# Kernel tuning notes

Hardware: AMD Instinct MI355X
Metric: run time of the kernel (lower is better)

The kernel has to match this reference:

```python
import jax, jax.numpy as jnp
import numpy as np

B, T, D, NH = 4, 2048, 768, 12
DH = D // NH
NEG = -100000.0  # module uses masked_fill with -100000.0, not -inf


def setup_inputs() -> dict:
    key = jax.random.key(0)
    ks = jax.random.split(key, 9)
    s = 1.0 / np.sqrt(D)
    return {
        "x": jax.random.normal(ks[0], (B, T, D), jnp.float32),
        "wq": jax.random.normal(ks[1], (D, D), jnp.float32) * s,
        "bq": jax.random.normal(ks[2], (D,), jnp.float32) * 0.02,
        "wk": jax.random.normal(ks[3], (D, D), jnp.float32) * s,
        "bk": jax.random.normal(ks[4], (D,), jnp.float32) * 0.02,
        "wv": jax.random.normal(ks[5], (D, D), jnp.float32) * s,
        "bv": jax.random.normal(ks[6], (D,), jnp.float32) * 0.02,
        "wo": jax.random.normal(ks[7], (D, D), jnp.float32) * s,
        "bo": jax.random.normal(ks[8], (D,), jnp.float32) * 0.02,
    }


def reference(x, wq, bq, wk, bk, wv, bv, wo, bo):
    Bx, Tx, E = x.shape
    # torch Linear: y = x @ W.T + b, weight shape [out, in]
    def heads(w, b):
        return (x @ w.T + b).reshape(Bx, Tx, NH, DH).transpose(0, 2, 1, 3)  # [B,nh,T,dh]
    Q, K, V = heads(wq, bq), heads(wk, bk), heads(wv, bv)
    scale = 1.0 / jnp.sqrt(jnp.float32(DH))
    QK = jnp.einsum("bhqd,bhkd->bhqk", Q, K) * scale  # [B,nh,T,T]
    causal = jnp.tril(jnp.ones((Tx, Tx), dtype=bool))
    QK = jnp.where(causal, QK, NEG)
    A = jax.nn.softmax(QK, axis=-1)  # attn_dropout p=0 (eval)
    Z = jnp.einsum("bhqk,bhkd->bhqd", A, V)
    Z = Z.transpose(0, 2, 1, 3).reshape(Bx, Tx, E)
    return Z @ wo.T + bo  # resid_dropout p=0 (eval)
```

## Files before the change

kernel.cpp:

```cpp
#include <hip/hip_runtime.h>


#define B_ 4
#define T_ 2048
#define D_ 768
#define NH_ 12
#define DH_ 64
#define M_ (B_ * T_)

typedef __attribute__((ext_vector_type(8))) short bf16x8;
typedef __attribute__((ext_vector_type(4))) float f32x4;
typedef __attribute__((ext_vector_type(16))) float f32x16;
typedef __attribute__((ext_vector_type(4))) unsigned int u32x4;

__device__ __forceinline__ unsigned short f2bf(float f) {
  unsigned int u = __builtin_bit_cast(unsigned int, f);
  u += 0x7FFFu + ((u >> 16) & 1u);
  return (unsigned short)(u >> 16);
}

__device__ __forceinline__ void async16(const void* g, void* l) {
  __builtin_amdgcn_global_load_lds(
      (const __attribute__((address_space(1))) unsigned int*)g,
      (__attribute__((address_space(3))) unsigned int*)l, 16, 0, 0);
}

#define RAW_BARRIER()                         \
  do {                                        \
    asm volatile("" ::: "memory");            \
    __builtin_amdgcn_s_barrier();             \
    asm volatile("" ::: "memory");            \
  } while (0)

__global__ void cvt_kernel(const float* __restrict__ x, const float* __restrict__ wq,
                           const float* __restrict__ wk, const float* __restrict__ wv,
                           const float* __restrict__ wo,
                           unsigned short* __restrict__ xb, unsigned short* __restrict__ wqb,
                           unsigned short* __restrict__ wkb, unsigned short* __restrict__ wvb,
                           unsigned short* __restrict__ wob) {
  const float* src; unsigned short* dst; int n4;
  switch (blockIdx.y) {
    case 0: src = x;  dst = xb;  n4 = M_ * D_ / 4; break;
    case 1: src = wq; dst = wqb; n4 = D_ * D_ / 4; break;
    case 2: src = wk; dst = wkb; n4 = D_ * D_ / 4; break;
    case 3: src = wv; dst = wvb; n4 = D_ * D_ / 4; break;
    default: src = wo; dst = wob; n4 = D_ * D_ / 4; break;
  }
  int stride = gridDim.x * blockDim.x;
  for (int i = blockIdx.x * blockDim.x + threadIdx.x; i < n4; i += stride) {
    float4 v = ((const float4*)src)[i];
    ushort4 o;
    o.x = f2bf(v.x); o.y = f2bf(v.y); o.z = f2bf(v.z); o.w = f2bf(v.w);
    ((ushort4*)dst)[i] = o;
  }
}

__global__ __launch_bounds__(512, 4) void gemm_kernel(
    const unsigned short* __restrict__ A,
    const unsigned short* __restrict__ W0, const unsigned short* __restrict__ W1,
    const unsigned short* __restrict__ W2,
    const float* __restrict__ bias0, const float* __restrict__ bias1,
    const float* __restrict__ bias2,
    void* out0, void* out1, void* out2,
    float s0, int K, int qkv) {
  __shared__ __align__(16) char lds[73728];

  int bid = blockIdx.x;
  int xcd = bid & 7, g = bid >> 3;
  int mt, nt;
  if (qkv) { mt = xcd + (g / 9) * 8; nt = g % 9; }
  else     { mt = xcd + (g / 3) * 8; nt = g % 3; }
  int y  = qkv ? nt / 3 : 0;
  int nW = qkv ? nt % 3 : nt;
  const unsigned short* W = y == 0 ? W0 : (y == 1 ? W1 : W2);
  const float* bias = y == 0 ? bias0 : (y == 1 ? bias1 : bias2);
  void* outp = y == 0 ? out0 : (y == 1 ? out1 : out2);
  float scl = (qkv && y == 0) ? s0 : 1.0f;
  int mode = qkv ? ((y == 2) ? 2 : 1) : 0;

  int tid = threadIdx.x, lane = tid & 63, wid = tid >> 6;
  int l15 = lane & 15, l4 = lane >> 4;
  int wm = wid >> 2, wn = wid & 3;
  int m0 = mt << 7, n0w = nW << 8;

  int aRow, aCol;
  {
    int row = wid * 16 + (lane >> 2);
    int colE = (lane & 3) * 8;
    aRow = row;
    aCol = colE ^ (((row >> 1) & 3) << 3);
  }
  int bRow[2], bCol[2];
#pragma unroll
  for (int c = 0; c < 2; ++c) {
    int u = c * 8 + wid;
    int row = u * 16 + (lane >> 2);
    int colE = (lane & 3) * 8;
    bRow[c] = row;
    bCol[c] = colE ^ (((row >> 1) & 3) << 3);
  }

  int aoff[4], boff[4];
#pragma unroll
  for (int mf = 0; mf < 4; ++mf) {
    int row = wm * 64 + mf * 16 + l15;
    aoff[mf] = row * 64 + ((l4 * 16) ^ (((row >> 1) & 3) << 4));
  }
#pragma unroll
  for (int nf = 0; nf < 4; ++nf) {
    int row = wn * 64 + nf * 16 + l15;
    boff[nf] = 8192 + row * 64 + ((l4 * 16) ^ (((row >> 1) & 3) << 4));
  }

  const unsigned short* Wb = W + (size_t)n0w * K;

#define ISSUE_TILE(kt, slot)                                                       \
  do {                                                                             \
    async16(A + (size_t)(m0 + aRow) * K + (kt) + aCol, (slot) + wid * 1024);       \
    _Pragma("unroll") for (int c = 0; c < 2; ++c)                                  \
      async16(Wb + (size_t)bRow[c] * K + (kt) + bCol[c],                           \
              (slot) + 8192 + (c * 8 + wid) * 1024);                               \
  } while (0)

  f32x4 acc[4][4] = {};
  char* b0 = lds;
  char* b1 = lds + 24576;
  char* b2 = lds + 49152;

  ISSUE_TILE(0, b0);
  ISSUE_TILE(32, b1);

  int NT = K >> 5;
#pragma unroll 1
  for (int t = 0; t < NT; ++t) {
    if (t + 1 < NT) asm volatile("s_waitcnt vmcnt(3)" ::: "memory");
    else            asm volatile("s_waitcnt vmcnt(0)" ::: "memory");
    RAW_BARRIER();
    if (t + 2 < NT) ISSUE_TILE((t + 2) << 5, b2);
    bf16x8 af[4], bfr[4];
#pragma unroll
    for (int mf = 0; mf < 4; ++mf) af[mf] = *(const bf16x8*)(b0 + aoff[mf]);
#pragma unroll
    for (int nf = 0; nf < 4; ++nf) bfr[nf] = *(const bf16x8*)(b0 + boff[nf]);
    __builtin_amdgcn_s_setprio(1);
#pragma unroll
    for (int mf = 0; mf < 4; ++mf)
#pragma unroll
      for (int nf = 0; nf < 4; ++nf)
        acc[mf][nf] = __builtin_amdgcn_mfma_f32_16x16x32_bf16(af[mf], bfr[nf], acc[mf][nf], 0, 0, 0);
    __builtin_amdgcn_s_setprio(0);
    char* tmp = b0; b0 = b1; b1 = b2; b2 = tmp;
  }
#undef ISSUE_TILE

  if (mode == 2) {
#pragma unroll
    for (int nf = 0; nf < 4; ++nf) {
      int colW = n0w + wn * 64 + nf * 16 + l15;
      float bv = bias[colW];
      int h = colW >> 6, d = colW & 63;
#pragma unroll
      for (int mf = 0; mf < 4; ++mf) {
        int rbase = m0 + wm * 64 + mf * 16 + l4 * 4;
        int bb = rbase >> 11, tt = rbase & (T_ - 1);
        ushort4 o;
        o.x = f2bf(acc[mf][nf][0] + bv);
        o.y = f2bf(acc[mf][nf][1] + bv);
        o.z = f2bf(acc[mf][nf][2] + bv);
        o.w = f2bf(acc[mf][nf][3] + bv);
        *(ushort4*)((unsigned short*)outp + ((size_t)(bb * NH_ + h) * DH_ + d) * T_ + tt) = o;
      }
    }
  } else {
#pragma unroll
    for (int nf = 0; nf < 4; ++nf) {
      int colW = n0w + wn * 64 + nf * 16 + l15;
      float bv = bias[colW];
#pragma unroll
      for (int mf = 0; mf < 4; ++mf) {
        int rbase = m0 + wm * 64 + mf * 16 + l4 * 4;
#pragma unroll
        for (int r = 0; r < 4; ++r) {
          float v = (acc[mf][nf][r] + bv) * scl;
          size_t idx = (size_t)(rbase + r) * D_ + colW;
          if (mode == 1) ((unsigned short*)outp)[idx] = f2bf(v);
          else           ((float*)outp)[idx] = v;
        }
      }
    }
  }
}

__global__ __launch_bounds__(256, 2) void attn_kernel(
    const unsigned short* __restrict__ Q, const unsigned short* __restrict__ Kg,
    const unsigned short* __restrict__ VT, unsigned short* __restrict__ Z) {
  __shared__ __align__(16) char lds[57344];

  int tid = threadIdx.x, lane = tid & 63, w = tid >> 6;
  int l31 = lane & 31, hi = lane >> 5;
  int bid = blockIdx.x;
  int xcd = bid & 7, g = bid >> 3;
  int qt = 15 - g / 6;
  int bh = xcd + (g % 6) * 8;
  int b = bh / NH_, h = bh % NH_;
  int q0 = qt * 128;
  int qrow = q0 + w * 32 + l31;

  const unsigned short* Qb = Q + (size_t)(b * T_) * D_ + h * DH_;
  const unsigned short* Kb = Kg + (size_t)(b * T_) * D_ + h * DH_;
  const unsigned short* VTb = VT + (size_t)(b * NH_ + h) * DH_ * T_;

  bf16x8 qf[4];
#pragma unroll
  for (int s = 0; s < 4; ++s)
    qf[s] = *(const bf16x8*)(Qb + (size_t)qrow * D_ + s * 16 + hi * 8);

  int sRow[2], sCol[2];
#pragma unroll
  for (int c = 0; c < 2; ++c) {
    int pos = ((c * 4 + w) * 64 + lane) * 8;
    int row = pos >> 6, colE = pos & 63;
    sRow[c] = row;
    sCol[c] = colE ^ ((row & 7) << 3);
  }

  int koff[2][4];
#pragma unroll
  for (int n = 0; n < 2; ++n)
#pragma unroll
    for (int s = 0; s < 4; ++s) {
      int row = n * 32 + l31;
      koff[n][s] = row * 128 + ((s * 32 + hi * 16) ^ ((row & 7) << 4));
    }

  f32x16 zt[2] = {};
  float l_run = 0.f;
  int ntiles = 2 * qt + 2;

#pragma unroll
  for (int c = 0; c < 2; ++c) {
    async16(Kb + (size_t)sRow[c] * D_ + sCol[c], lds + 0 + (c * 4 + w) * 1024);
    async16(VTb + (size_t)sRow[c] * T_ + sCol[c], lds + 16384 + (c * 4 + w) * 1024);
  }

#define ATTN_TILE(KCUR, VCUR, KNXT, VNXT)                                              \
  do {                                                                                 \
    __syncthreads();          \
    if (t + 1 < ntiles) {                                                              \
      int kv1 = (t + 1) * 64;                                                          \
      _Pragma("unroll") for (int c = 0; c < 2; ++c) {                                  \
        async16(Kb + (size_t)(kv1 + sRow[c]) * D_ + sCol[c],                           \
                lds + KNXT + (c * 4 + w) * 1024);                                      \
        async16(VTb + (size_t)sRow[c] * T_ + kv1 + sCol[c],                            \
                lds + VNXT + (c * 4 + w) * 1024);                                      \
      }                                                                                \
    }                                                                                  \
    f32x16 st[2];                                                                      \
    __builtin_amdgcn_s_setprio(1);                                                     \
    _Pragma("unroll") for (int n = 0; n < 2; ++n) {                                    \
      f32x16 a = {};                                                                   \
      _Pragma("unroll") for (int s = 0; s < 4; ++s) {                                  \
        bf16x8 kf = *(const bf16x8*)(lds + KCUR + koff[n][s]);                         \
        a = __builtin_amdgcn_mfma_f32_32x32x16_bf16(kf, qf[s], a, 0, 0, 0);            \
      }                                                                                \
      st[n] = a;                                                                       \
    }                                                                                  \
    __builtin_amdgcn_s_setprio(0);                                                     \
    if (t >= 2 * qt) {                            \
      int kvb = t * 64;                                                                \
      _Pragma("unroll") for (int n = 0; n < 2; ++n)                                    \
        _Pragma("unroll") for (int m = 0; m < 4; ++m)                                  \
          _Pragma("unroll") for (int c2 = 0; c2 < 4; ++c2) {                           \
            int kv = kvb + n * 32 + m * 8 + hi * 4 + c2;                               \
            if (kv > qrow) st[n][m * 4 + c2] = -1e30f;                                 \
          }                                                                            \
    }                                                                                  \
    bf16x8 pb[4];                                                                      \
    _Pragma("unroll") for (int n = 0; n < 2; ++n) {                                    \
      float u[16];                                                                     \
      _Pragma("unroll") for (int r = 0; r < 16; ++r) {                                 \
        u[r] = __builtin_amdgcn_exp2f(st[n][r]);                                       \
        l_run += u[r];                                                                 \
      }                                                                                \
      _Pragma("unroll") for (int hf = 0; hf < 2; ++hf) {                               \
        unsigned int A0, A1, B0, B1;                                                   \
        asm("v_cvt_pk_bf16_f32 %0, %1, %2" : "=v"(A0) : "v"(u[hf*8+0]), "v"(u[hf*8+1]));\
        asm("v_cvt_pk_bf16_f32 %0, %1, %2" : "=v"(A1) : "v"(u[hf*8+2]), "v"(u[hf*8+3]));\
        asm("v_cvt_pk_bf16_f32 %0, %1, %2" : "=v"(B0) : "v"(u[hf*8+4]), "v"(u[hf*8+5]));\
        asm("v_cvt_pk_bf16_f32 %0, %1, %2" : "=v"(B1) : "v"(u[hf*8+6]), "v"(u[hf*8+7]));\
        asm("v_permlane32_swap_b32 %0, %1" : "+v"(A0), "+v"(B0));                      \
        asm("v_permlane32_swap_b32 %0, %1" : "+v"(A1), "+v"(B1));                      \
        u32x4 pk; pk[0] = A0; pk[1] = A1; pk[2] = B0; pk[3] = B1;                      \
        pb[n * 2 + hf] = __builtin_bit_cast(bf16x8, pk);                               \
      }                                                                                \
    }                                                                                  \
    __builtin_amdgcn_s_setprio(1);                                                     \
    _Pragma("unroll") for (int dt = 0; dt < 2; ++dt) {                                 \
      _Pragma("unroll") for (int s = 0; s < 4; ++s) {                                  \
        bf16x8 vf = *(const bf16x8*)(lds + VCUR + koff[dt][s]);                        \
        zt[dt] = __builtin_amdgcn_mfma_f32_32x32x16_bf16(vf, pb[s], zt[dt], 0, 0, 0);  \
      }                                                                                \
    }                                                                                  \
    __builtin_amdgcn_s_setprio(0);                                                     \
  } while (0)

#pragma unroll 1
  for (int t = 0; t < ntiles; ++t) {
    if ((t & 1) == 0) {
      ATTN_TILE(0, 16384, 8192, 24576);
    } else {
      ATTN_TILE(8192, 24576, 0, 16384);
    }
  }
#undef ATTN_TILE

  l_run += __shfl_xor(l_run, 32);
  float inv = __builtin_amdgcn_rcpf(l_run);
  unsigned short* Zrow = Z + (size_t)(b * T_ + qrow) * D_ + h * DH_;
#pragma unroll
  for (int dt = 0; dt < 2; ++dt)
#pragma unroll
    for (int m = 0; m < 4; ++m) {
      ushort4 o;
      o.x = f2bf(zt[dt][m * 4 + 0] * inv);
      o.y = f2bf(zt[dt][m * 4 + 1] * inv);
      o.z = f2bf(zt[dt][m * 4 + 2] * inv);
      o.w = f2bf(zt[dt][m * 4 + 3] * inv);
      *(ushort4*)(Zrow + dt * 32 + m * 8 + hi * 4) = o;
    }
}

extern "C" void kernel_launch(void* const* d_in, const int* in_sizes, int n_in,
                              void* d_out, int out_size, void* d_ws, size_t ws_size,
                              hipStream_t stream) {
  (void)in_sizes; (void)n_in; (void)out_size; (void)ws_size;
  const float* x  = (const float*)d_in[0];
  const float* wq = (const float*)d_in[1];
  const float* bq = (const float*)d_in[2];
  const float* wk = (const float*)d_in[3];
  const float* bk = (const float*)d_in[4];
  const float* wv = (const float*)d_in[5];
  const float* bv = (const float*)d_in[6];
  const float* wo = (const float*)d_in[7];
  const float* bo = (const float*)d_in[8];

  char* ws = (char*)d_ws;
  const size_t XB = (size_t)M_ * D_ * 2;
  const size_t WB = (size_t)D_ * D_ * 2;
  unsigned short* xb  = (unsigned short*)(ws);
  unsigned short* wqb = (unsigned short*)(ws + XB);
  unsigned short* wkb = (unsigned short*)(ws + XB + WB);
  unsigned short* wvb = (unsigned short*)(ws + XB + 2 * WB);
  unsigned short* wob = (unsigned short*)(ws + XB + 3 * WB);
  unsigned short* Qb  = (unsigned short*)(ws + XB + 4 * WB);
  unsigned short* Kb  = (unsigned short*)(ws + XB + 4 * WB + XB);
  unsigned short* VTb = (unsigned short*)(ws + XB + 4 * WB + 2 * XB);
  unsigned short* Zb  = xb;

  const float SCALE_Q = 0.125f * 1.44269504f;

  cvt_kernel<<<dim3(1024, 5), 256, 0, stream>>>(x, wq, wk, wv, wo, xb, wqb, wkb, wvb, wob);
  gemm_kernel<<<dim3(576), 512, 0, stream>>>(
      xb, wqb, wkb, wvb, bq, bk, bv, Qb, Kb, VTb, SCALE_Q, D_, 1);
  attn_kernel<<<dim3(768), 256, 0, stream>>>(Qb, Kb, VTb, Zb);
  gemm_kernel<<<dim3(192), 512, 0, stream>>>(
      Zb, wob, wob, wob, bo, bo, bo, d_out, d_out, d_out, 1.0f, D_, 0);
}
```

Baseline: 117.1 us.

## Load GEMM weight fragments directly to registers, double-buffer only A in LDS

The GEMM now stages only the activation tile in LDS with two buffers instead of three, and each wave loads its weight (B) fragments straight from global memory into registers, double-buffered across k-steps. This cuts LDS use from 72KB to 16KB and drops the launch_bounds minimum-occupancy hint. The aim is to save LDS bandwidth and shared-memory capacity, allowing more blocks per CU. In exchange, the weight rows are loaded redundantly by each wave without LDS sharing, the prefetch depth drops from two tiles to one, and register pressure rises.

```diff
diff --git a/kernel.cpp b/kernel.cpp
--- a/kernel.cpp
+++ b/kernel.cpp
@@ -55,7 +55,7 @@
   }
 }
 
-__global__ __launch_bounds__(512, 4) void gemm_kernel(
+__global__ __launch_bounds__(512) void gemm_kernel(
     const unsigned short* __restrict__ A,
     const unsigned short* __restrict__ W0, const unsigned short* __restrict__ W1,
     const unsigned short* __restrict__ W2,
@@ -63,7 +63,7 @@
     const float* __restrict__ bias2,
     void* out0, void* out1, void* out2,
     float s0, int K, int qkv) {
-  __shared__ __align__(16) char lds[73728];
+  __shared__ __align__(16) char lds[16384];
 
   int bid = blockIdx.x;
   int xcd = bid & 7, g = bid >> 3;
@@ -90,68 +90,62 @@
     aRow = row;
     aCol = colE ^ (((row >> 1) & 3) << 3);
   }
-  int bRow[2], bCol[2];
-#pragma unroll
-  for (int c = 0; c < 2; ++c) {
-    int u = c * 8 + wid;
-    int row = u * 16 + (lane >> 2);
-    int colE = (lane & 3) * 8;
-    bRow[c] = row;
-    bCol[c] = colE ^ (((row >> 1) & 3) << 3);
-  }
-
-  int aoff[4], boff[4];
+  int aoff[4];
 #pragma unroll
   for (int mf = 0; mf < 4; ++mf) {
     int row = wm * 64 + mf * 16 + l15;
     aoff[mf] = row * 64 + ((l4 * 16) ^ (((row >> 1) & 3) << 4));
   }
-#pragma unroll
-  for (int nf = 0; nf < 4; ++nf) {
-    int row = wn * 64 + nf * 16 + l15;
-    boff[nf] = 8192 + row * 64 + ((l4 * 16) ^ (((row >> 1) & 3) << 4));
-  }
-
-  const unsigned short* Wb = W + (size_t)n0w * K;
-
-#define ISSUE_TILE(kt, slot)                                                       \
+
+  const unsigned short* Wfrag = W + (size_t)(n0w + wn * 64 + l15) * K + l4 * 8;
+  const size_t nstep = (size_t)16 * K;
+
+#define ISSUE_A(kt, slot) \
+  async16(A + (size_t)(m0 + aRow) * K + (kt) + aCol, (slot) + wid * 1024)
+
+  f32x4 acc[4][4] = {};
+  char* slot0 = lds;
+  char* slot1 = lds + 8192;
+  bf16x8 bA[4], bB[4];
+
+  ISSUE_A(0, slot0);
+#pragma unroll
+  for (int nf = 0; nf < 4; ++nf)
+    bA[nf] = *(const bf16x8*)(Wfrag + nf * nstep);
+
+  int NT = K >> 5;
+
+#define STEP(t, CUR, NXT, BCUR, BNXT)                                              \
   do {                                                                             \
-    async16(A + (size_t)(m0 + aRow) * K + (kt) + aCol, (slot) + wid * 1024);       \
-    _Pragma("unroll") for (int c = 0; c < 2; ++c)                                  \
-      async16(Wb + (size_t)bRow[c] * K + (kt) + bCol[c],                           \
-              (slot) + 8192 + (c * 8 + wid) * 1024);                               \
+    RAW_BARRIER();            \
+    if ((t) + 1 < NT) {                                                            \
+      int kt1 = ((t) + 1) << 5;                                                    \
+      ISSUE_A(kt1, NXT);                                                           \
+      _Pragma("unroll") for (int nf = 0; nf < 4; ++nf)                             \
+        BNXT[nf] = *(const bf16x8*)(Wfrag + nf * nstep + kt1);                     \
+      asm volatile("s_waitcnt vmcnt(5)" ::: "memory");         \
+    } else {                                                                       \
+      asm volatile("s_waitcnt vmcnt(0)" ::: "memory");             \
+    }                                                                              \
+    RAW_BARRIER();                              \
+    bf16x8 af[4];                                                                  \
+    _Pragma("unroll") for (int mf = 0; mf < 4; ++mf)                               \
+      af[mf] = *(const bf16x8*)((CUR) + aoff[mf]);                                 \
+    __builtin_amdgcn_s_setprio(1);                                                 \
+    _Pragma("unroll") for (int mf = 0; mf < 4; ++mf)                               \
+      _Pragma("unroll") for (int nf = 0; nf < 4; ++nf)                             \
+        acc[mf][nf] = __builtin_amdgcn_mfma_f32_16x16x32_bf16(                     \
+            af[mf], BCUR[nf], acc[mf][nf], 0, 0, 0);                               \
+    __builtin_amdgcn_s_setprio(0);                                                 \
   } while (0)
 
-  f32x4 acc[4][4] = {};
-  char* b0 = lds;
-  char* b1 = lds + 24576;
-  char* b2 = lds + 49152;
-
-  ISSUE_TILE(0, b0);
-  ISSUE_TILE(32, b1);
-
-  int NT = K >> 5;
 #pragma unroll 1
-  for (int t = 0; t < NT; ++t) {
-    if (t + 1 < NT) asm volatile("s_waitcnt vmcnt(3)" ::: "memory");
-    else            asm volatile("s_waitcnt vmcnt(0)" ::: "memory");
-    RAW_BARRIER();
-    if (t + 2 < NT) ISSUE_TILE((t + 2) << 5, b2);
-    bf16x8 af[4], bfr[4];
-#pragma unroll
-    for (int mf = 0; mf < 4; ++mf) af[mf] = *(const bf16x8*)(b0 + aoff[mf]);
-#pragma unroll
-    for (int nf = 0; nf < 4; ++nf) bfr[nf] = *(const bf16x8*)(b0 + boff[nf]);
-    __builtin_amdgcn_s_setprio(1);
-#pragma unroll
-    for (int mf = 0; mf < 4; ++mf)
-#pragma unroll
-      for (int nf = 0; nf < 4; ++nf)
-        acc[mf][nf] = __builtin_amdgcn_mfma_f32_16x16x32_bf16(af[mf], bfr[nf], acc[mf][nf], 0, 0, 0);
-    __builtin_amdgcn_s_setprio(0);
-    char* tmp = b0; b0 = b1; b1 = b2; b2 = tmp;
-  }
-#undef ISSUE_TILE
+  for (int t = 0; t < NT; t += 2) {
+    STEP(t, slot0, slot1, bA, bB);
+    STEP(t + 1, slot1, slot0, bB, bA);
+  }
+#undef STEP
+#undef ISSUE_A
 
   if (mode == 2) {
 #pragma unroll
```

After: 184.8 us. 57.8% more time.

## Use four-slot K/V ring buffer in attention, syncing every two tiles

Applied to the files above, without the earlier changes.

Replaces the double-buffered K/V staging in the attention kernel with a four-slot ring buffer. Two tiles are prefetched at a time, and the block-wide barrier now runs only every other tile. This is meant to halve barrier overhead and give the async loads more lead time. In exchange, LDS use grows from 56 KB to 64 KB per block, which may limit occupancy. The loop relies on ntiles always being even.

```diff
diff --git a/kernel.cpp b/kernel.cpp
--- a/kernel.cpp
+++ b/kernel.cpp
@@ -69,7 +69,7 @@
   int xcd = bid & 7, g = bid >> 3;
   int mt, nt;
   if (qkv) { mt = xcd + (g / 9) * 8; nt = g % 9; }
-  else     { mt = xcd + (g / 3) * 8; nt = g % 3; }
+  else     { mt = xcd + (g / 3) * 8;  nt = g % 3; }
   int y  = qkv ? nt / 3 : 0;
   int nW = qkv ? nt % 3 : nt;
   const unsigned short* W = y == 0 ? W0 : (y == 1 ? W1 : W2);
@@ -194,7 +194,7 @@
 __global__ __launch_bounds__(256, 2) void attn_kernel(
     const unsigned short* __restrict__ Q, const unsigned short* __restrict__ Kg,
     const unsigned short* __restrict__ VT, unsigned short* __restrict__ Z) {
-  __shared__ __align__(16) char lds[57344];
+  __shared__ __align__(16) char lds[65536];
 
   int tid = threadIdx.x, lane = tid & 63, w = tid >> 6;
   int l31 = lane & 31, hi = lane >> 5;
@@ -237,82 +237,95 @@
   float l_run = 0.f;
   int ntiles = 2 * qt + 2;
 
-#pragma unroll
-  for (int c = 0; c < 2; ++c) {
-    async16(Kb + (size_t)sRow[c] * D_ + sCol[c], lds + 0 + (c * 4 + w) * 1024);
-    async16(VTb + (size_t)sRow[c] * T_ + sCol[c], lds + 16384 + (c * 4 + w) * 1024);
-  }
-
-#define ATTN_TILE(KCUR, VCUR, KNXT, VNXT)                                              \
-  do {                                                                                 \
-    __syncthreads();          \
-    if (t + 1 < ntiles) {                                                              \
-      int kv1 = (t + 1) * 64;                                                          \
-      _Pragma("unroll") for (int c = 0; c < 2; ++c) {                                  \
-        async16(Kb + (size_t)(kv1 + sRow[c]) * D_ + sCol[c],                           \
-                lds + KNXT + (c * 4 + w) * 1024);                                      \
-        async16(VTb + (size_t)sRow[c] * T_ + kv1 + sCol[c],                            \
-                lds + VNXT + (c * 4 + w) * 1024);                                      \
-      }                                                                                \
-    }                                                                                  \
-    f32x16 st[2];                                                                      \
-    __builtin_amdgcn_s_setprio(1);                                                     \
-    _Pragma("unroll") for (int n = 0; n < 2; ++n) {                                    \
-      f32x16 a = {};                                                                   \
-      _Pragma("unroll") for (int s = 0; s < 4; ++s) {                                  \
-        bf16x8 kf = *(const bf16x8*)(lds + KCUR + koff[n][s]);                         \
-        a = __builtin_amdgcn_mfma_f32_32x32x16_bf16(kf, qf[s], a, 0, 0, 0);            \
-      }                                                                                \
-      st[n] = a;                                                                       \
-    }                                                                                  \
-    __builtin_amdgcn_s_setprio(0);                                                     \
-    if (t >= 2 * qt) {                            \
-      int kvb = t * 64;                                                                \
-      _Pragma("unroll") for (int n = 0; n < 2; ++n)                                    \
-        _Pragma("unroll") for (int m = 0; m < 4; ++m)                                  \
-          _Pragma("unroll") for (int c2 = 0; c2 < 4; ++c2) {                           \
-            int kv = kvb + n * 32 + m * 8 + hi * 4 + c2;                               \
-            if (kv > qrow) st[n][m * 4 + c2] = -1e30f;                                 \
-          }                                                                            \
-    }                                                                                  \
-    bf16x8 pb[4];                                                                      \
-    _Pragma("unroll") for (int n = 0; n < 2; ++n) {                                    \
-      float u[16];                                                                     \
-      _Pragma("unroll") for (int r = 0; r < 16; ++r) {                                 \
-        u[r] = __builtin_amdgcn_exp2f(st[n][r]);                                       \
-        l_run += u[r];                                                                 \
-      }                                                                                \
-      _Pragma("unroll") for (int hf = 0; hf < 2; ++hf) {                               \
-        unsigned int A0, A1, B0, B1;                                                   \
-        asm("v_cvt_pk_bf16_f32 %0, %1, %2" : "=v"(A0) : "v"(u[hf*8+0]), "v"(u[hf*8+1]));\
-        asm("v_cvt_pk_bf16_f32 %0, %1, %2" : "=v"(A1) : "v"(u[hf*8+2]), "v"(u[hf*8+3]));\
-        asm("v_cvt_pk_bf16_f32 %0, %1, %2" : "=v"(B0) : "v"(u[hf*8+4]), "v"(u[hf*8+5]));\
-        asm("v_cvt_pk_bf16_f32 %0, %1, %2" : "=v"(B1) : "v"(u[hf*8+6]), "v"(u[hf*8+7]));\
-        asm("v_permlane32_swap_b32 %0, %1" : "+v"(A0), "+v"(B0));                      \
-        asm("v_permlane32_swap_b32 %0, %1" : "+v"(A1), "+v"(B1));                      \
-        u32x4 pk; pk[0] = A0; pk[1] = A1; pk[2] = B0; pk[3] = B1;                      \
-        pb[n * 2 + hf] = __builtin_bit_cast(bf16x8, pk);                               \
-      }                                                                                \
-    }                                                                                  \
-    __builtin_amdgcn_s_setprio(1);                                                     \
-    _Pragma("unroll") for (int dt = 0; dt < 2; ++dt) {                                 \
-      _Pragma("unroll") for (int s = 0; s < 4; ++s) {                                  \
-        bf16x8 vf = *(const bf16x8*)(lds + VCUR + koff[dt][s]);                        \
-        zt[dt] = __builtin_amdgcn_mfma_f32_32x32x16_bf16(vf, pb[s], zt[dt], 0, 0, 0);  \
-      }                                                                                \
-    }                                                                                  \
-    __builtin_amdgcn_s_setprio(0);                                                     \
+#define STAGE(tt)                                                                  \
+  do {                                                                             \
+    int kv0 = (tt) * 64;                                                           \
+    int kb = ((tt) & 3) << 13;                                                     \
+    _Pragma("unroll") for (int c = 0; c < 2; ++c) {                                \
+      async16(Kb + (size_t)(kv0 + sRow[c]) * D_ + sCol[c],                         \
+              lds + kb + (c * 4 + w) * 1024);                                      \
+      async16(VTb + (size_t)sRow[c] * T_ + kv0 + sCol[c],                          \
+              lds + 32768 + kb + (c * 4 + w) * 1024);                              \
+    }                                                                              \
   } while (0)
+
+  STAGE(0);
+  STAGE(1);
 
 #pragma unroll 1
   for (int t = 0; t < ntiles; ++t) {
     if ((t & 1) == 0) {
-      ATTN_TILE(0, 16384, 8192, 24576);
-    } else {
-      ATTN_TILE(8192, 24576, 0, 16384);
-    }
-  }
-#undef ATTN_TILE
+      __syncthreads();
+      if (t + 2 < ntiles) {
+        STAGE(t + 2);
+        STAGE(t + 3);
+      }
+    }
+    const char* kbase = lds + ((t & 3) << 13);
+    const char* vbase = lds + 32768 + ((t & 3) << 13);
+
+    f32x16 st[2];
+    __builtin_amdgcn_s_setprio(1);
+#pragma unroll
+    for (int n = 0; n < 2; ++n) {
+      f32x16 a = {};
+#pragma unroll
+      for (int s = 0; s < 4; ++s) {
+        bf16x8 kf = *(const bf16x8*)(kbase + koff[n][s]);
+        a = __builtin_amdgcn_mfma_f32_32x32x16_bf16(kf, qf[s], a, 0, 0, 0);
+      }
+      st[n] = a;
+    }
+    __builtin_amdgcn_s_setprio(0);
+
+    if (t >= 2 * qt) {
+      int kvb = t * 64;
+#pragma unroll
+      for (int n = 0; n < 2; ++n)
+#pragma unroll
+        for (int m = 0; m < 4; ++m)
+#pragma unroll
+          for (int c2 = 0; c2 < 4; ++c2) {
+            int kv = kvb + n * 32 + m * 8 + hi * 4 + c2;
+            if (kv > qrow) st[n][m * 4 + c2] = -1e30f;
+          }
+    }
+
+    bf16x8 pb[4];
+#pragma unroll
+    for (int n = 0; n < 2; ++n) {
+      float u[16];
+#pragma unroll
+      for (int r = 0; r < 16; ++r) {
+        u[r] = __builtin_amdgcn_exp2f(st[n][r]);
+        l_run += u[r];
+      }
+#pragma unroll
+      for (int hf = 0; hf < 2; ++hf) {
+        unsigned int A0, A1, B0, B1;
+        asm("v_cvt_pk_bf16_f32 %0, %1, %2" : "=v"(A0) : "v"(u[hf*8+0]), "v"(u[hf*8+1]));
+        asm("v_cvt_pk_bf16_f32 %0, %1, %2" : "=v"(A1) : "v"(u[hf*8+2]), "v"(u[hf*8+3]));
+        asm("v_cvt_pk_bf16_f32 %0, %1, %2" : "=v"(B0) : "v"(u[hf*8+4]), "v"(u[hf*8+5]));
+        asm("v_cvt_pk_bf16_f32 %0, %1, %2" : "=v"(B1) : "v"(u[hf*8+6]), "v"(u[hf*8+7]));
+        asm("v_permlane32_swap_b32 %0, %1" : "+v"(A0), "+v"(B0));
+        asm("v_permlane32_swap_b32 %0, %1" : "+v"(A1), "+v"(B1));
+        u32x4 pk; pk[0] = A0; pk[1] = A1; pk[2] = B0; pk[3] = B1;
+        pb[n * 2 + hf] = __builtin_bit_cast(bf16x8, pk);
+      }
+    }
+
+    __builtin_amdgcn_s_setprio(1);
+#pragma unroll
+    for (int dt = 0; dt < 2; ++dt) {
+#pragma unroll
+      for (int s = 0; s < 4; ++s) {
+        bf16x8 vf = *(const bf16x8*)(vbase + koff[dt][s]);
+        zt[dt] = __builtin_amdgcn_mfma_f32_32x32x16_bf16(vf, pb[s], zt[dt], 0, 0, 0);
+      }
+    }
+    __builtin_amdgcn_s_setprio(0);
+  }
+#undef STAGE
 
   l_run += __shfl_xor(l_run, 32);
   float inv = __builtin_amdgcn_rcpf(l_run);
```

Result: no change. 115.0 us, median of 2 (-1.8%).
